# Kernel optimization log

Measured on AMD Instinct MI355X. Metric: run time of the kernel, lower is better.

The kernel has to match this reference:

```python
import jax, jax.numpy as jnp
import numpy as np

D_MODEL = 1024
NUM_HEADS = 16


def setup_inputs() -> dict:
    key = jax.random.key(0)
    ks = jax.random.split(key, 6)
    B, N, L, C = 16, 1024, 120, D_MODEL
    s = 0.02
    return {
        "x": jax.random.normal(ks[0], (B, N, C), jnp.float32),
        "cond": jax.random.normal(ks[1], (B, L, C), jnp.float32),
        "mask": jax.random.randint(ks[2], (B, L), 0, 2, jnp.int32),
        "Wq": jax.random.normal(ks[3], (C, C), jnp.float32) * s,
        "bq": jnp.zeros((C,), jnp.float32),
        "Wkv": jax.random.normal(ks[4], (2 * C, C), jnp.float32) * s,
        "bkv": jnp.zeros((2 * C,), jnp.float32),
        "Wp": jax.random.normal(ks[5], (C, C), jnp.float32) * s,
        "bp": jnp.zeros((C,), jnp.float32),
    }


def reference(x, cond, mask, Wq, bq, Wkv, bkv, Wp, bp):
    B, N, C = x.shape
    H = NUM_HEADS
    Dh = C // H
    scale = Dh ** (-0.5)
    # q: (B,H,N,Dh)
    q = (x @ Wq.T + bq).reshape(B, N, H, Dh).transpose(0, 2, 1, 3)
    # kv: (2,B,H,L,Dh)
    L = cond.shape[1]
    kv = (cond @ Wkv.T + bkv).reshape(B, L, 2, H, Dh).transpose(2, 0, 3, 1, 4)
    k, v = kv[0], kv[1]
    # attention scores (B,H,N,L)
    attn = jnp.einsum("bhnd,bhld->bhnl", q, k) * scale
    attn = jnp.where(mask[:, None, None, :] == 0, -jnp.inf, attn)
    attn = jax.nn.softmax(attn, axis=-1)
    out = jnp.einsum("bhnl,bhld->bhnd", attn, v)  # (B,H,N,Dh)
    out = out.transpose(0, 2, 1, 3).reshape(B, N, C)
    return out @ Wp.T + bp
```

## Files before the change

### kernel.cpp

```cpp
#include <hip/hip_runtime.h>

typedef unsigned short u16;
typedef unsigned int u32;
typedef float f32x4 __attribute__((ext_vector_type(4)));
typedef __bf16 bf16x8 __attribute__((ext_vector_type(8)));
typedef u32 u32x4 __attribute__((ext_vector_type(4)));
typedef u16 u16x4 __attribute__((ext_vector_type(4)));

#define NB 16
#define NSEQ 1024
#define NL 120
#define NLP 128
#define NC 1024
#define NH 16
#define NDH 64
#define KSP 72
#define VTP 136

__device__ __forceinline__ u16 f2bf(float f) {
  u32 u = __float_as_uint(f);
  return (u16)((u + 0x7fffu + ((u >> 16) & 1u)) >> 16);
}

__device__ __forceinline__ void gld_lds16(const void* g, void* l) {
  __builtin_amdgcn_global_load_lds(
      (const __attribute__((address_space(1))) void*)g,
      (__attribute__((address_space(3))) void*)l, 16, 0, 0);
}

__global__ __launch_bounds__(256) void cast_all(
    const float* __restrict__ x, u16* __restrict__ xb,
    const float* __restrict__ cond, u16* __restrict__ condb,
    const float* __restrict__ Wq, u16* __restrict__ Wqb,
    const float* __restrict__ Wkv, u16* __restrict__ Wkvb,
    const float* __restrict__ Wp, u16* __restrict__ Wpb) {
  int bk = blockIdx.x;
  const float* src;
  u16* dst;
  if (bk < 16384) { src = x; dst = xb; }
  else if (bk < 18304) { src = cond; dst = condb; bk -= 16384; }
  else if (bk < 19328) { src = Wq; dst = Wqb; bk -= 18304; }
  else if (bk < 21376) { src = Wkv; dst = Wkvb; bk -= 19328; }
  else { src = Wp; dst = Wpb; bk -= 21376; }
  size_t i = ((size_t)bk * 256 + threadIdx.x) * 4;
  f32x4 v = *(const f32x4*)(src + i);
  u16x4 o;
  o.x = f2bf(v.x); o.y = f2bf(v.y); o.z = f2bf(v.z); o.w = f2bf(v.w);
  *(u16x4*)(dst + i) = o;
}

template <bool OUT_F32>
__global__ __launch_bounds__(256) void gemm_bt(
    const u16* __restrict__ A, const u16* __restrict__ Bt,
    const float* __restrict__ bias, void* __restrict__ Cout,
    int M, int Nn, int K) {
  __shared__ u16 As[128 * 32];
  __shared__ u16 Bs[128 * 32];
  const int mt = M >> 7;
  const int bm = (int)blockIdx.x % mt;
  const int bn = (int)blockIdx.x / mt;
  const int m0 = bm << 7, n0 = bn << 7;
  const int tid = threadIdx.x;
  const int w = tid >> 6, lane = tid & 63;
  const int wm = (w & 1) << 6, wn = (w >> 1) << 6;
  const int quad = lane >> 4, l15 = lane & 15;

  f32x4 acc[4][4];
#pragma unroll
  for (int i = 0; i < 4; ++i)
#pragma unroll
    for (int j = 0; j < 4; ++j) acc[i][j] = (f32x4){0.f, 0.f, 0.f, 0.f};

  const int r0 = tid >> 2;
  const int cb = ((((tid & 3) - (r0 >> 1)) & 3)) << 3;
  const u16* aP = A + (size_t)(m0 + r0) * K + cb;
  const u16* bP = Bt + (size_t)(n0 + r0) * K + cb;
  u16* asDst = &As[r0 * 32 + ((tid & 3) << 3)];
  u16* bsDst = &Bs[r0 * 32 + ((tid & 3) << 3)];

  const int sw = ((quad + (l15 >> 1)) & 3) << 3;

  for (int k0 = 0; k0 < K; k0 += 32) {
    __syncthreads();
    gld_lds16(aP + k0, asDst);
    gld_lds16(aP + (size_t)64 * K + k0, asDst + 64 * 32);
    gld_lds16(bP + k0, bsDst);
    gld_lds16(bP + (size_t)64 * K + k0, bsDst + 64 * 32);
    __syncthreads();

    bf16x8 af[4], bfr[4];
#pragma unroll
    for (int i = 0; i < 4; ++i)
      af[i] = *(const bf16x8*)&As[(wm + i * 16 + l15) * 32 + sw];
#pragma unroll
    for (int j = 0; j < 4; ++j)
      bfr[j] = *(const bf16x8*)&Bs[(wn + j * 16 + l15) * 32 + sw];
#pragma unroll
    for (int i = 0; i < 4; ++i)
#pragma unroll
      for (int j = 0; j < 4; ++j)
        acc[i][j] =
            __builtin_amdgcn_mfma_f32_16x16x32_bf16(af[i], bfr[j], acc[i][j], 0, 0, 0);
  }

#pragma unroll
  for (int j = 0; j < 4; ++j) {
    const int col = n0 + wn + j * 16 + l15;
    const float bv = bias[col];
#pragma unroll
    for (int i = 0; i < 4; ++i) {
      const int row = m0 + wm + i * 16 + quad * 4;
#pragma unroll
      for (int r = 0; r < 4; ++r) {
        const float v = acc[i][j][r] + bv;
        if (OUT_F32)
          ((float*)Cout)[(size_t)(row + r) * Nn + col] = v;
        else
          ((u16*)Cout)[(size_t)(row + r) * Nn + col] = f2bf(v);
      }
    }
  }
}

__global__ __launch_bounds__(256) void attn(
    const u16* __restrict__ Qb, const u16* __restrict__ KVb,
    const int* __restrict__ mask, u16* __restrict__ Ob) {
  __shared__ u16 Ks[NLP * KSP];
  __shared__ u16 Vt[NDH * VTP];
  __shared__ float mb[NLP];
  __shared__ u16 pb[4][16 * VTP];

  const int chunk = (int)blockIdx.x & 3;
  const int h = ((int)blockIdx.x >> 2) & 15;
  const int b = (int)blockIdx.x >> 6;
  const int tid = threadIdx.x;
  const int w = tid >> 6, lane = tid & 63;
  const int quad = lane >> 4, l15 = lane & 15;
  const u16* kvbase = KVb + (size_t)b * NL * 2 * NC;

  for (int i = tid; i < NLP * 8; i += 256) {
    const int l = i >> 3, c8 = (i & 7) * 8;
    u32x4 z = {0u, 0u, 0u, 0u};
    u32x4 v = (l < NL) ? *(const u32x4*)(kvbase + (size_t)l * 2 * NC + h * NDH + c8) : z;
    *(u32x4*)&Ks[l * KSP + c8] = v;
  }
  u16* vstage = &pb[0][0];
  for (int i = tid; i < NL * 8; i += 256) {
    const int l = i >> 3, c8 = (i & 7) * 8;
    *(u32x4*)&vstage[l * NDH + c8] =
        *(const u32x4*)(kvbase + (size_t)l * 2 * NC + NC + h * NDH + c8);
  }
  for (int i = tid; i < NLP; i += 256)
    mb[i] = (i < NL && mask[b * NL + i] != 0) ? 0.0f : -1e30f;
  __syncthreads();
  for (int i = tid; i < NDH * NLP; i += 256) {
    const int d = i >> 7, l = i & 127;
    Vt[d * VTP + l] = (l < NL) ? vstage[l * NDH + d] : (u16)0;
  }
  __syncthreads();

  const float scale = 0.125f;
  for (int it = 0; it < 4; ++it) {
    const int q0 = chunk * 256 + it * 64 + w * 16;
    const u16* qptr = Qb + (size_t)(b * NSEQ + q0 + l15) * NC + h * NDH + quad * 8;
    const bf16x8 a0 = *(const bf16x8*)qptr;
    const bf16x8 a1 = *(const bf16x8*)(qptr + 32);

    f32x4 s[8];
#pragma unroll
    for (int kt = 0; kt < 8; ++kt) {
      const u16* kb = &Ks[(kt * 16 + l15) * KSP + quad * 8];
      const bf16x8 b0 = *(const bf16x8*)kb;
      const bf16x8 b1 = *(const bf16x8*)(kb + 32);
      f32x4 t = {0.f, 0.f, 0.f, 0.f};
      t = __builtin_amdgcn_mfma_f32_16x16x32_bf16(a0, b0, t, 0, 0, 0);
      t = __builtin_amdgcn_mfma_f32_16x16x32_bf16(a1, b1, t, 0, 0, 0);
      s[kt] = t;
    }
#pragma unroll
    for (int kt = 0; kt < 8; ++kt) {
      const float mbv = mb[kt * 16 + l15];
#pragma unroll
      for (int r = 0; r < 4; ++r) s[kt][r] = s[kt][r] * scale + mbv;
    }
    float sum[4];
#pragma unroll
    for (int r = 0; r < 4; ++r) {
      float m = s[0][r];
#pragma unroll
      for (int kt = 1; kt < 8; ++kt) m = fmaxf(m, s[kt][r]);
      m = fmaxf(m, __shfl_xor(m, 1));
      m = fmaxf(m, __shfl_xor(m, 2));
      m = fmaxf(m, __shfl_xor(m, 4));
      m = fmaxf(m, __shfl_xor(m, 8));
      float su = 0.f;
#pragma unroll
      for (int kt = 0; kt < 8; ++kt) {
        s[kt][r] = __expf(s[kt][r] - m);
        su += s[kt][r];
      }
      su += __shfl_xor(su, 1);
      su += __shfl_xor(su, 2);
      su += __shfl_xor(su, 4);
      su += __shfl_xor(su, 8);
      sum[r] = su;
    }
#pragma unroll
    for (int r = 0; r < 4; ++r) {
      const float inv = 1.0f / sum[r];
#pragma unroll
      for (int kt = 0; kt < 8; ++kt)
        pb[w][(quad * 4 + r) * VTP + kt * 16 + l15] = f2bf(s[kt][r] * inv);
    }
#pragma unroll
    for (int ntl = 0; ntl < 4; ++ntl) {
      f32x4 o = {0.f, 0.f, 0.f, 0.f};
#pragma unroll
      for (int kt = 0; kt < 4; ++kt) {
        const bf16x8 pa = *(const bf16x8*)&pb[w][l15 * VTP + kt * 32 + quad * 8];
        const bf16x8 vb = *(const bf16x8*)&Vt[(ntl * 16 + l15) * VTP + kt * 32 + quad * 8];
        o = __builtin_amdgcn_mfma_f32_16x16x32_bf16(pa, vb, o, 0, 0, 0);
      }
#pragma unroll
      for (int r = 0; r < 4; ++r)
        Ob[(size_t)(b * NSEQ + q0 + quad * 4 + r) * NC + h * NDH + ntl * 16 + l15] =
            f2bf(o[r]);
    }
  }
}

extern "C" void kernel_launch(void* const* d_in, const int* in_sizes, int n_in,
                              void* d_out, int out_size, void* d_ws, size_t ws_size,
                              hipStream_t stream) {
  const float* x = (const float*)d_in[0];
  const float* cond = (const float*)d_in[1];
  const int* mask = (const int*)d_in[2];
  const float* Wq = (const float*)d_in[3];
  const float* bq = (const float*)d_in[4];
  const float* Wkv = (const float*)d_in[5];
  const float* bkv = (const float*)d_in[6];
  const float* Wp = (const float*)d_in[7];
  const float* bp = (const float*)d_in[8];

  char* ws = (char*)d_ws;
  u16* xb = (u16*)(ws + 0);
  u16* condb = (u16*)(ws + 33554432);
  u16* Wqb = (u16*)(ws + 37486592);
  u16* Wkvb = (u16*)(ws + 39583744);
  u16* Wpb = (u16*)(ws + 43778048);
  u16* Qb = (u16*)(ws + 45875200);
  u16* KVb = (u16*)(ws + 79429632);
  u16* Ob = xb;

  cast_all<<<22400, 256, 0, stream>>>(x, xb, cond, condb, Wq, Wqb, Wkv, Wkvb, Wp, Wpb);

  gemm_bt<false><<<128 * 8, 256, 0, stream>>>(xb, Wqb, bq, Qb, 16384, 1024, 1024);
  gemm_bt<false><<<15 * 16, 256, 0, stream>>>(condb, Wkvb, bkv, KVb, 1920, 2048, 1024);
  attn<<<1024, 256, 0, stream>>>(Qb, KVb, mask, Ob);
  gemm_bt<true><<<128 * 8, 256, 0, stream>>>(Ob, Wpb, bp, d_out, 16384, 1024, 1024);
}
```

Measured before the change: 329.9 us.

## Replace large GEMMs with 256x256 double-buffered pipelined MFMA kernel

```diff
diff --git a/kernel.cpp b/kernel.cpp
--- a/kernel.cpp
+++ b/kernel.cpp
@@ -27,6 +27,18 @@
       (const __attribute__((address_space(1))) void*)g,
       (__attribute__((address_space(3))) void*)l, 16, 0, 0);
 }
+
+#define SBAR()                               \
+  do {                                       \
+    __builtin_amdgcn_sched_barrier(0);       \
+    __builtin_amdgcn_s_barrier();            \
+    __builtin_amdgcn_sched_barrier(0);       \
+  } while (0)
+#define VMW(n)                                          \
+  do {                                                  \
+    __builtin_amdgcn_sched_barrier(0);                  \
+    asm volatile("s_waitcnt vmcnt(" #n ")" ::: "memory"); \
+  } while (0)
 
 __global__ __launch_bounds__(256) void cast_all(
     const float* __restrict__ x, u16* __restrict__ xb,
@@ -122,6 +134,141 @@
   }
 }
 
+template <bool OUT_F32>
+__global__ __launch_bounds__(512, 2) void gemm256(
+    const u16* __restrict__ A, const u16* __restrict__ Bt,
+    const float* __restrict__ bias, void* __restrict__ Cout,
+    int M, int Nn, int K) {
+  __shared__ u16 S[2][2][2][8192];
+
+  const int bid = (int)blockIdx.x;
+  const int nwg = (M >> 8) * (Nn >> 8);
+  const int cpx = nwg >> 3;
+  const int swz = (bid & 7) * cpx + (bid >> 3);
+  const int mt = M >> 8;
+  const int bm = swz % mt, bn = swz / mt;
+  const int m0 = bm << 8, n0 = bn << 8;
+
+  const int tid = threadIdx.x;
+  const int w = tid >> 6, lane = tid & 63;
+  const int quad = lane >> 4, l15 = lane & 15;
+  const int wr = w & 1, wc = w >> 1;
+
+  const int srow = tid >> 3;
+  const int xoff = (((tid & 7) ^ (srow & 7)) << 3);
+  const u16* aB0 = A + (size_t)(m0 + srow) * K + xoff;
+  const u16* bB0 = Bt + (size_t)(n0 + srow) * K + xoff;
+  const size_t rowK64 = (size_t)64 * K;
+  const size_t rowK128 = (size_t)128 * K;
+
+  auto STAGE = [&](int ab, int buf, int half, int t) {
+    const u16* g = (ab ? bB0 : aB0) + half * rowK128 + t * 64;
+    u16* d = &S[ab][buf][half][0] + tid * 8;
+    gld_lds16(g, d);
+    gld_lds16(g + rowK64, d + 4096);
+  };
+
+  const int c0 = ((quad << 4) ^ ((l15 & 7) << 4));
+  const int c1 = c0 ^ 64;
+  const int arow = (wr * 64 + l15) * 128;
+  const int brow = (wc * 32 + l15) * 128;
+
+  bf16x8 af[4][2], bfl[2][2], bfh[2][2];
+  auto LDA = [&](int buf, int rh) {
+    const char* base = (const char*)&S[0][buf][rh][0] + arow;
+#pragma unroll
+    for (int f = 0; f < 4; ++f) {
+      af[f][0] = *(const bf16x8*)(base + f * 2048 + c0);
+      af[f][1] = *(const bf16x8*)(base + f * 2048 + c1);
+    }
+  };
+  auto LDB = [&](bf16x8(&bf)[2][2], int buf, int ch) {
+    const char* base = (const char*)&S[1][buf][ch][0] + brow;
+#pragma unroll
+    for (int g = 0; g < 2; ++g) {
+      bf[g][0] = *(const bf16x8*)(base + g * 2048 + c0);
+      bf[g][1] = *(const bf16x8*)(base + g * 2048 + c1);
+    }
+  };
+
+  f32x4 a_ll[4][2], a_lh[4][2], a_hh[4][2], a_hl[4][2];
+#pragma unroll
+  for (int f = 0; f < 4; ++f)
+#pragma unroll
+    for (int g = 0; g < 2; ++g) {
+      a_ll[f][g] = (f32x4){0.f, 0.f, 0.f, 0.f};
+      a_lh[f][g] = (f32x4){0.f, 0.f, 0.f, 0.f};
+      a_hh[f][g] = (f32x4){0.f, 0.f, 0.f, 0.f};
+      a_hl[f][g] = (f32x4){0.f, 0.f, 0.f, 0.f};
+    }
+
+  auto MM = [&](f32x4(&acc)[4][2], bf16x8(&bf)[2][2]) {
+    __builtin_amdgcn_s_setprio(1);
+#pragma unroll
+    for (int f = 0; f < 4; ++f)
+#pragma unroll
+      for (int g = 0; g < 2; ++g) {
+        acc[f][g] = __builtin_amdgcn_mfma_f32_16x16x32_bf16(af[f][0], bf[g][0],
+                                                            acc[f][g], 0, 0, 0);
+        acc[f][g] = __builtin_amdgcn_mfma_f32_16x16x32_bf16(af[f][1], bf[g][1],
+                                                            acc[f][g], 0, 0, 0);
+      }
+    __builtin_amdgcn_s_setprio(0);
+  };
+
+  const int NT = K >> 6;
+  const int NIT = K >> 7;
+
+  STAGE(0, 0, 0, 0); STAGE(0, 0, 1, 0); STAGE(1, 0, 0, 0); STAGE(1, 0, 1, 0);
+  STAGE(0, 1, 0, 1); STAGE(1, 1, 1, 1);
+  VMW(4);
+  SBAR();
+
+#pragma unroll 1
+  for (int it = 0; it < NIT; ++it) {
+    const int t1 = 2 * it + 1;
+    int t2 = 2 * it + 2; if (t2 > NT - 1) t2 = NT - 1;
+    int t3 = 2 * it + 3; if (t3 > NT - 1) t3 = NT - 1;
+    LDA(0, 0); LDB(bfl, 0, 0); STAGE(1, 1, 0, t1);
+    SBAR(); MM(a_ll, bfl); SBAR();
+    LDB(bfh, 0, 1); STAGE(0, 1, 1, t1);
+    SBAR(); MM(a_lh, bfh); VMW(6); SBAR();
+    LDA(0, 1); STAGE(0, 0, 0, t2);
+    SBAR(); MM(a_hh, bfh); SBAR();
+    STAGE(1, 0, 1, t2);
+    SBAR(); MM(a_hl, bfl); VMW(6); SBAR();
+    LDA(1, 0); LDB(bfl, 1, 0); STAGE(1, 0, 0, t2);
+    SBAR(); MM(a_ll, bfl); SBAR();
+    LDB(bfh, 1, 1); STAGE(0, 0, 1, t2);
+    SBAR(); MM(a_lh, bfh); VMW(6); SBAR();
+    LDA(1, 1); STAGE(0, 1, 0, t3);
+    SBAR(); MM(a_hh, bfh); SBAR();
+    STAGE(1, 1, 1, t3);
+    SBAR(); MM(a_hl, bfl); VMW(6); SBAR();
+  }
+
+  auto EPI = [&](f32x4(&acc)[4][2], int rh, int ch) {
+#pragma unroll
+    for (int g = 0; g < 2; ++g) {
+      const int col = n0 + ch * 128 + wc * 32 + g * 16 + l15;
+      const float bv = bias[col];
+#pragma unroll
+      for (int f = 0; f < 4; ++f) {
+        const int row = m0 + rh * 128 + wr * 64 + f * 16 + quad * 4;
+#pragma unroll
+        for (int r = 0; r < 4; ++r) {
+          const float v = acc[f][g][r] + bv;
+          if (OUT_F32)
+            ((float*)Cout)[(size_t)(row + r) * Nn + col] = v;
+          else
+            ((u16*)Cout)[(size_t)(row + r) * Nn + col] = f2bf(v);
+        }
+      }
+    }
+  };
+  EPI(a_ll, 0, 0); EPI(a_lh, 0, 1); EPI(a_hh, 1, 1); EPI(a_hl, 1, 0);
+}
+
 __global__ __launch_bounds__(256) void attn(
     const u16* __restrict__ Qb, const u16* __restrict__ KVb,
     const int* __restrict__ mask, u16* __restrict__ Ob) {
@@ -254,8 +401,8 @@
 
   cast_all<<<22400, 256, 0, stream>>>(x, xb, cond, condb, Wq, Wqb, Wkv, Wkvb, Wp, Wpb);
 
-  gemm_bt<false><<<128 * 8, 256, 0, stream>>>(xb, Wqb, bq, Qb, 16384, 1024, 1024);
+  gemm256<false><<<256, 512, 0, stream>>>(xb, Wqb, bq, Qb, 16384, 1024, 1024);
   gemm_bt<false><<<15 * 16, 256, 0, stream>>>(condb, Wkvb, bkv, KVb, 1920, 2048, 1024);
   attn<<<1024, 256, 0, stream>>>(Qb, KVb, mask, Ob);
-  gemm_bt<true><<<128 * 8, 256, 0, stream>>>(Ob, Wpb, bp, d_out, 16384, 1024, 1024);
-}
+  gemm256<true><<<256, 512, 0, stream>>>(Ob, Wpb, bp, d_out, 16384, 1024, 1024);
+}
```

New measurement: 292.5 us. -11.4%, faster.
